# Optimization experiments

Hardware: AMD Instinct MI355X
Metric: run time of the kernel (lower is better)

## Reference

```python
import jax, jax.numpy as jnp
import numpy as np

B, S_DEC, S_ENC, D, H = 2, 2048, 2048, 1024, 16
HD = D // H  # 64


def setup_inputs() -> dict:
    key = jax.random.key(0)
    ks = jax.random.split(key, 12)
    s = 0.02
    return {
        "dec_hidden_state": jax.random.normal(ks[0], (B, S_DEC, D), jnp.float32),
        "enc_hidden_state": jax.random.normal(ks[1], (B, S_ENC, D), jnp.float32),
        "mask": jnp.ones((B, S_ENC, S_DEC), jnp.int32),
        "Wq": jax.random.normal(ks[2], (H, D, HD), jnp.float32) * s,
        "bq": jax.random.normal(ks[3], (H, HD), jnp.float32) * s,
        "Wk": jax.random.normal(ks[4], (H, D, HD), jnp.float32) * s,
        "bk": jax.random.normal(ks[5], (H, HD), jnp.float32) * s,
        "Wv": jax.random.normal(ks[6], (H, D, HD), jnp.float32) * s,
        "bv": jax.random.normal(ks[7], (H, HD), jnp.float32) * s,
        "Wo": jax.random.normal(ks[8], (D, D), jnp.float32) * s,
        "bo": jax.random.normal(ks[9], (D,), jnp.float32) * s,
    }


def reference(dec_hidden_state, enc_hidden_state, mask, Wq, bq, Wk, bk, Wv, bv, Wo, bo):
    # NOTE: original module swaps args: query <- enc_hidden_state, key/value <- dec_hidden_state.
    # q: [B,H,S_enc,HD], k/v: [B,H,S_dec,HD]
    q = jnp.einsum("bqd,hdk->bhqk", enc_hidden_state, Wq) + bq[None, :, None, :]
    k = jnp.einsum("bsd,hdk->bhsk", dec_hidden_state, Wk) + bk[None, :, None, :]
    v = jnp.einsum("bsd,hdk->bhsk", dec_hidden_state, Wv) + bv[None, :, None, :]
    scores = jnp.einsum("bhqk,bhsk->bhqs", q, k) / jnp.sqrt(jnp.asarray(HD, q.dtype))
    scores = jnp.where(mask[:, None, :, :] == 0, jnp.asarray(-jnp.inf, scores.dtype), scores)
    weights = jax.nn.softmax(scores, axis=-1)
    attn = jnp.einsum("bhqs,bhsk->bhqk", weights, v)  # [B,H,S_enc,HD]
    # concat heads along last dim (same order as torch.cat over head list)
    attn = jnp.transpose(attn, (0, 2, 1, 3)).reshape(B, S_ENC, D)
    return attn @ Wo + bo
```

## Files before the change

kernel.cpp:

```cpp
#include <hip/hip_runtime.h>
#include <math.h>
#include <stdint.h>


typedef unsigned short ushort_t;
typedef __attribute__((ext_vector_type(8))) short short8;
typedef __attribute__((ext_vector_type(4))) float floatx4;

__device__ __forceinline__ ushort_t f2bf(float x){
  unsigned u = __float_as_uint(x);
  u += 0x7fffu + ((u >> 16) & 1u);
  return (ushort_t)(u >> 16);
}
__device__ __forceinline__ unsigned pk2bf(float a, float b){
#if __has_builtin(__builtin_amdgcn_cvt_pk_bf16_f32)
  typedef __attribute__((ext_vector_type(2))) __bf16 bf2_t;
  bf2_t r = __builtin_amdgcn_cvt_pk_bf16_f32(a, b);
  return *(unsigned*)&r;
#else
  return (unsigned)f2bf(a) | ((unsigned)f2bf(b) << 16);
#endif
}
__device__ __forceinline__ floatx4 mfma16(short8 a, short8 b, floatx4 c){
  return __builtin_amdgcn_mfma_f32_16x16x32_bf16(a, b, c, 0, 0, 0);
}

__global__ __launch_bounds__(256)
void prep_kernel(const float* __restrict__ enc, const float* __restrict__ dec,
                 const float* __restrict__ Wq, const float* __restrict__ Wk,
                 const float* __restrict__ Wv, const float* __restrict__ Wo,
                 const int* __restrict__ mask,
                 ushort_t* __restrict__ encb, ushort_t* __restrict__ decb,
                 ushort_t* __restrict__ WqT, ushort_t* __restrict__ WkT,
                 ushort_t* __restrict__ WvT, ushort_t* __restrict__ WoT,
                 unsigned long long* __restrict__ mb)
{
  __shared__ float t[64][65];
  const int bx = blockIdx.x, tid = threadIdx.x;
  if (bx < 8192){
    const float* src = (bx < 4096) ? enc : dec;
    ushort_t*    dst = (bx < 4096) ? encb : decb;
    int i = ((bx & 4095) * 256 + tid) * 4;
    const float4 v = *(const float4*)(src + i);
    unsigned long long p = (unsigned long long)f2bf(v.x)
                         | ((unsigned long long)f2bf(v.y) << 16)
                         | ((unsigned long long)f2bf(v.z) << 32)
                         | ((unsigned long long)f2bf(v.w) << 48);
    *(unsigned long long*)(dst + i) = p;
  } else if (bx < 8960){
    const int id = bx - 8192;
    const int zz = id >> 4, yy = id & 15;
    const int which = zz >> 4, head = zz & 15;
    const float* src = (which == 0) ? Wq : (which == 1) ? Wk : Wv;
    ushort_t*    dst = (which == 0) ? WqT : (which == 1) ? WkT : WvT;
    const long sb = (long)head * 65536;
    const int r0 = yy * 64;
    #pragma unroll
    for (int i = 0; i < 16; i++){
      int idx = i*256 + tid;
      int r = idx >> 6, c = idx & 63;
      t[r][c] = src[sb + (long)(r0 + r)*64 + c];
    }
    __syncthreads();
    #pragma unroll
    for (int i = 0; i < 16; i++){
      int idx = i*256 + tid;
      int cr = idx >> 6, rc = idx & 63;
      dst[sb + (long)cr*1024 + r0 + rc] = f2bf(t[rc][cr]);
    }
  } else if (bx < 9216){
    const int id = bx - 8960;
    const int r0 = (id >> 4) * 64, c0 = (id & 15) * 64;
    #pragma unroll
    for (int i = 0; i < 16; i++){
      int idx = i*256 + tid;
      int r = idx >> 6, c = idx & 63;
      t[r][c] = Wo[(long)(r0 + r)*1024 + c0 + c];
    }
    __syncthreads();
    #pragma unroll
    for (int i = 0; i < 16; i++){
      int idx = i*256 + tid;
      int cr = idx >> 6, rc = idx & 63;
      WoT[(long)(c0 + cr)*1024 + r0 + rc] = f2bf(t[rc][cr]);
    }
  } else {
    long gid = (long)(bx - 9216) * 256 + tid;
    unsigned long long bal = __ballot(mask[gid] != 0);
    if ((tid & 63) == 0) mb[gid >> 6] = bal;
  }
}

__global__ __launch_bounds__(256, 3)
void gemm_qkv_kernel(const ushort_t* __restrict__ encb, const ushort_t* __restrict__ decb,
                     const ushort_t* __restrict__ WqT, const ushort_t* __restrict__ WkT,
                     const ushort_t* __restrict__ WvT,
                     const float* __restrict__ bq, const float* __restrict__ bk,
                     const float* __restrict__ bv,
                     ushort_t* __restrict__ Qb, ushort_t* __restrict__ Kbf,
                     ushort_t* __restrict__ Vtb)
{
  __shared__ ushort_t At[2*4096];
  __shared__ ushort_t Bt[2*4096];
  const int tid = threadIdx.x;
  const int wave = tid >> 6, lane = tid & 63;
  const int quad = lane >> 4, l16 = lane & 15;
  const int z = blockIdx.z;
  const ushort_t *A, *BT; const float* bias; ushort_t* outp;
  int m0, n0; long outAdj = 0;
  float qs = 1.0f;
  if (z == 0){ A = encb; BT = WqT; bias = bq; outp = Qb;  m0 = blockIdx.x*128; n0 = blockIdx.y*128;
               qs = 0.18033688011112042f; }
  else if (z == 1){ A = decb; BT = WkT; bias = bk; outp = Kbf; m0 = blockIdx.x*128; n0 = blockIdx.y*128; }
  else {
    int id = blockIdx.x*8 + blockIdx.y;
    int vb = id >> 7, rem = id & 127;
    m0 = ((rem >> 4) & 7) * 128; n0 = (rem & 15) * 128;
    A = WvT; BT = decb + (long)vb*2097152; bias = bv; outp = Vtb; outAdj = (long)vb*2097152;
  }
  const int K = 1024;

  const int c0 = tid, c1 = 256 + tid;
  const ushort_t* gA0 = A  + (long)(m0 + (c0 >> 2))*K + (c0 & 3)*8;
  const ushort_t* gA1 = A  + (long)(m0 + (c1 >> 2))*K + (c1 & 3)*8;
  const ushort_t* gB0 = BT + (long)(n0 + (c0 >> 2))*K + (c0 & 3)*8;
  const ushort_t* gB1 = BT + (long)(n0 + (c1 >> 2))*K + (c1 & 3)*8;

  floatx4 acc[4][4];
  #pragma unroll
  for (int mt = 0; mt < 4; mt++)
    #pragma unroll
    for (int nt = 0; nt < 4; nt++)
      acc[mt][nt] = (floatx4){0.f, 0.f, 0.f, 0.f};

  short8 rA0 = *(const short8*)gA0;  gA0 += 32;
  short8 rA1 = *(const short8*)gA1;  gA1 += 32;
  short8 rB0 = *(const short8*)gB0;  gB0 += 32;
  short8 rB1 = *(const short8*)gB1;  gB1 += 32;

  const int moff = (wave & 1) * 64, noff = (wave >> 1) * 64;
  int cur = 0;
  for (int k0 = 0; k0 < K; k0 += 32){
    *(short8*)&At[cur*4096 +        tid*8] = rA0;
    *(short8*)&At[cur*4096 + 2048 + tid*8] = rA1;
    *(short8*)&Bt[cur*4096 +        tid*8] = rB0;
    *(short8*)&Bt[cur*4096 + 2048 + tid*8] = rB1;
    __syncthreads();
    if (k0 + 32 < K){
      rA0 = *(const short8*)gA0;  gA0 += 32;
      rA1 = *(const short8*)gA1;  gA1 += 32;
      rB0 = *(const short8*)gB0;  gB0 += 32;
      rB1 = *(const short8*)gB1;  gB1 += 32;
    }
    short8 af[4], bfr[4];
    #pragma unroll
    for (int t = 0; t < 4; t++){
      af[t]  = *(const short8*)&At[cur*4096 + (moff + t*16 + l16)*32 + quad*8];
      bfr[t] = *(const short8*)&Bt[cur*4096 + (noff + t*16 + l16)*32 + quad*8];
    }
    #pragma unroll
    for (int mt = 0; mt < 4; mt++)
      #pragma unroll
      for (int nt = 0; nt < 4; nt++)
        acc[mt][nt] = mfma16(bfr[nt], af[mt], acc[mt][nt]);
    cur ^= 1;
  }

  #pragma unroll
  for (int mt = 0; mt < 4; mt++){
    #pragma unroll
    for (int nt = 0; nt < 4; nt++){
      floatx4 v = acc[mt][nt];
      if (z < 2){
        const int s   = m0 + moff + mt*16 + l16;
        const int ch0 = n0 + noff + nt*16 + quad*4;
        const float4 b4 = *(const float4*)&bias[ch0];
        uint2 pk;
        pk.x = pk2bf((v[0] + b4.x)*qs, (v[1] + b4.y)*qs);
        pk.y = pk2bf((v[2] + b4.z)*qs, (v[3] + b4.w)*qs);
        *(unsigned long long*)&outp[(long)s*1024 + ch0] = *(unsigned long long*)&pk;
      } else {
        const int ch = m0 + moff + mt*16 + l16;
        const int s0 = n0 + noff + nt*16 + quad*4;
        const float bb = bias[ch];
        uint2 pk;
        pk.x = pk2bf(v[0] + bb, v[1] + bb);
        pk.y = pk2bf(v[2] + bb, v[3] + bb);
        *(unsigned long long*)&outp[outAdj + (long)ch*2048 + s0] = *(unsigned long long*)&pk;
      }
    }
  }
}

__global__ __launch_bounds__(256, 2)
void gemm_o_kernel(const ushort_t* __restrict__ A, const ushort_t* __restrict__ BT,
                   const float* __restrict__ bias, float* __restrict__ outf)
{
  __shared__ ushort_t At[2*4096];
  __shared__ ushort_t Bt[2*2048];
  const int tid = threadIdx.x;
  const int wave = tid >> 6, lane = tid & 63;
  const int quad = lane >> 4, l16 = lane & 15;
  const int m0 = blockIdx.x * 128, n0 = blockIdx.y * 64;
  const int K = 1024;

  const int c0 = tid, c1 = 256 + tid;
  const ushort_t* gA0 = A  + (long)(m0 + (c0 >> 2))*K + (c0 & 3)*8;
  const ushort_t* gA1 = A  + (long)(m0 + (c1 >> 2))*K + (c1 & 3)*8;
  const ushort_t* gB0 = BT + (long)(n0 + (c0 >> 2))*K + (c0 & 3)*8;

  floatx4 acc[4][2];
  #pragma unroll
  for (int mt = 0; mt < 4; mt++)
    #pragma unroll
    for (int nt = 0; nt < 2; nt++)
      acc[mt][nt] = (floatx4){0.f, 0.f, 0.f, 0.f};

  short8 rA0 = *(const short8*)gA0;  gA0 += 32;
  short8 rA1 = *(const short8*)gA1;  gA1 += 32;
  short8 rB0 = *(const short8*)gB0;  gB0 += 32;

  const int moff = (wave & 1) * 64, noff = (wave >> 1) * 32;
  int cur = 0;
  for (int k0 = 0; k0 < K; k0 += 32){
    *(short8*)&At[cur*4096 +        tid*8] = rA0;
    *(short8*)&At[cur*4096 + 2048 + tid*8] = rA1;
    *(short8*)&Bt[cur*2048 +        tid*8] = rB0;
    __syncthreads();
    if (k0 + 32 < K){
      rA0 = *(const short8*)gA0;  gA0 += 32;
      rA1 = *(const short8*)gA1;  gA1 += 32;
      rB0 = *(const short8*)gB0;  gB0 += 32;
    }
    short8 af[4], bfr[2];
    #pragma unroll
    for (int t = 0; t < 4; t++)
      af[t]  = *(const short8*)&At[cur*4096 + (moff + t*16 + l16)*32 + quad*8];
    #pragma unroll
    for (int t = 0; t < 2; t++)
      bfr[t] = *(const short8*)&Bt[cur*2048 + (noff + t*16 + l16)*32 + quad*8];
    #pragma unroll
    for (int mt = 0; mt < 4; mt++)
      #pragma unroll
      for (int nt = 0; nt < 2; nt++)
        acc[mt][nt] = mfma16(bfr[nt], af[mt], acc[mt][nt]);
    cur ^= 1;
  }

  #pragma unroll
  for (int mt = 0; mt < 4; mt++){
    #pragma unroll
    for (int nt = 0; nt < 2; nt++){
      const int s   = m0 + moff + mt*16 + l16;
      const int ch0 = n0 + noff + nt*16 + quad*4;
      const float4 b4 = *(const float4*)&bias[ch0];
      float4 o;
      o.x = acc[mt][nt][0] + b4.x;
      o.y = acc[mt][nt][1] + b4.y;
      o.z = acc[mt][nt][2] + b4.z;
      o.w = acc[mt][nt][3] + b4.w;
      *(float4*)&outf[(long)s*1024 + ch0] = o;
    }
  }
}

#define SM_PB(zA_, zB_, wv_, lsum_, pb_)                              \
  {                                                                   \
    float p0 = __builtin_amdgcn_exp2f((zA_)[0]);                      \
    float p1 = __builtin_amdgcn_exp2f((zA_)[1]);                      \
    float p2 = __builtin_amdgcn_exp2f((zA_)[2]);                      \
    float p3 = __builtin_amdgcn_exp2f((zA_)[3]);                      \
    float p4 = __builtin_amdgcn_exp2f((zB_)[0]);                      \
    float p5 = __builtin_amdgcn_exp2f((zB_)[1]);                      \
    float p6 = __builtin_amdgcn_exp2f((zB_)[2]);                      \
    float p7 = __builtin_amdgcn_exp2f((zB_)[3]);                      \
    if (__builtin_expect(!uni, 0)){                                   \
      const int sh_ = quad*8;                                         \
      p0 = (((wv_) >> (sh_+0)) & 1u) ? p0 : 0.f;                      \
      p1 = (((wv_) >> (sh_+1)) & 1u) ? p1 : 0.f;                      \
      p2 = (((wv_) >> (sh_+2)) & 1u) ? p2 : 0.f;                      \
      p3 = (((wv_) >> (sh_+3)) & 1u) ? p3 : 0.f;                      \
      p4 = (((wv_) >> (sh_+4)) & 1u) ? p4 : 0.f;                      \
      p5 = (((wv_) >> (sh_+5)) & 1u) ? p5 : 0.f;                      \
      p6 = (((wv_) >> (sh_+6)) & 1u) ? p6 : 0.f;                      \
      p7 = (((wv_) >> (sh_+7)) & 1u) ? p7 : 0.f;                      \
    }                                                                 \
    lsum_ += ((p0 + p1) + (p2 + p3)) + ((p4 + p5) + (p6 + p7));       \
    unsigned pk0_ = pk2bf(p0, p1);                                    \
    unsigned pk1_ = pk2bf(p2, p3);                                    \
    unsigned pk2_ = pk2bf(p4, p5);                                    \
    unsigned pk3_ = pk2bf(p6, p7);                                    \
    unsigned tmp_[4] = {pk0_, pk1_, pk2_, pk3_};                      \
    __builtin_memcpy(&(pb_), tmp_, 16);                               \
  }

__global__ __launch_bounds__(512, 4)
void flash_attn_kernel(const ushort_t* __restrict__ Qp, const ushort_t* __restrict__ Kp,
                       const ushort_t* __restrict__ Vt, const unsigned* __restrict__ mb,
                       ushort_t* __restrict__ aout)
{
  __shared__ __align__(16) unsigned char smem_raw[73728];
  ushort_t* KBs = (ushort_t*)smem_raw;
  ushort_t* VBs = KBs + 2*2*4608;
  float* mO = (float*)smem_raw;
  float* mL = (float*)(smem_raw + 32768);

  const int tid = threadIdx.x, wave = tid >> 6, lane = tid & 63;
  const int quad = lane >> 4, l16 = lane & 15;
  const int shalf = wave >> 2, w = wave & 3;
  const int bh = blockIdx.x, qt = blockIdx.y;
  const int b = bh >> 4, h = bh & 15;

  const ushort_t* VB = Vt + (long)bh*131072;
  const int q0 = qt*128 + w*32;

  short8 qfA0, qfA1, qfB0, qfB1;
  {
    const long qrowA = ((long)b*2048 + q0 + l16)*1024 + h*64;
    qfA0 = *(const short8*)&Qp[qrowA +      quad*8];
    qfA1 = *(const short8*)&Qp[qrowA + 32 + quad*8];
    const long qrowB = qrowA + 16*1024;
    qfB0 = *(const short8*)&Qp[qrowB +      quad*8];
    qfB1 = *(const short8*)&Qp[qrowB + 32 + quad*8];
  }

  floatx4 accA[4], accB[4];
  #pragma unroll
  for (int ht = 0; ht < 4; ht++){
    accA[ht] = (floatx4){0.f,0.f,0.f,0.f};
    accB[ht] = (floatx4){0.f,0.f,0.f,0.f};
  }
  float lsA = 0.f, lsB = 0.f;

  const int htid = tid & 255;
  const int c0 = htid, c1 = 256 + htid;
  const int sr0 = c0 >> 3, sr1 = c1 >> 3;
  const int kr0 = (sr0 & 32) + ((sr0 & 4) << 2) + ((sr0 >> 3) & 3)*4 + (sr0 & 3);
  const int kr1 = (sr1 & 32) + ((sr1 & 4) << 2) + ((sr1 >> 3) & 3)*4 + (sr1 & 3);
  const long srow = (long)b*2048 + shalf*1024;
  const ushort_t* gK0 = Kp + (srow + sr0)*1024 + h*64 + (c0 & 7)*8;
  const ushort_t* gK1 = Kp + (srow + sr1)*1024 + h*64 + (c1 & 7)*8;
  const ushort_t* gV0 = VB + (long)sr0*2048 + shalf*1024 + (c0 & 7)*8;
  const ushort_t* gV1 = VB + (long)sr1*2048 + shalf*1024 + (c1 & 7)*8;
  ushort_t* Kh = KBs + shalf*2*4608;
  ushort_t* Vh = VBs + shalf*2*4608;
  const int ko0 = kr0*72 + (c0 & 7)*8;
  const int ko1 = kr1*72 + (c1 & 7)*8;
  const int vo0 = sr0*72 + (c0 & 7)*8;
  const int vo1 = sr1*72 + (c1 & 7)*8;

  const uint2* mb2 = (const uint2*)mb;
  const long mbase = (long)b*2048 + q0;

  short8 gk0 = *(const short8*)gK0;  gK0 += 65536;
  short8 gk1 = *(const short8*)gK1;  gK1 += 65536;
  short8 gv0 = *(const short8*)gV0;  gV0 += 64;
  short8 gv1 = *(const short8*)gV1;  gV1 += 64;

  int cur = 0;
  for (int st = 0; st < 16; st++){
    *(short8*)&Kh[cur*4608 + ko0] = gk0;
    *(short8*)&Kh[cur*4608 + ko1] = gk1;
    *(short8*)&Vh[cur*4608 + vo0] = gv0;
    *(short8*)&Vh[cur*4608 + vo1] = gv1;
    __syncthreads();
    if (st < 15){
      gk0 = *(const short8*)gK0;  gK0 += 65536;
      gk1 = *(const short8*)gK1;  gK1 += 65536;
      gv0 = *(const short8*)gV0;  gV0 += 64;
      gv1 = *(const short8*)gV1;  gV1 += 64;
    }
    const ushort_t* Kt = &Kh[cur*4608];
    const ushort_t* Vp = &Vh[cur*4608];

    const uint2 mwA = mb2[(mbase +      l16)*32 + shalf*16 + st];
    const uint2 mwB = mb2[(mbase + 16 + l16)*32 + shalf*16 + st];
    const bool uni = __all((mwA.x & mwA.y & mwB.x & mwB.y) == 0xFFFFFFFFu);

    #pragma unroll
    for (int c = 0; c < 2; c++){
      short8 kA0 = *(const short8*)&Kt[((c*2    )*16 + l16)*72 +      quad*8];
      short8 kA1 = *(const short8*)&Kt[((c*2    )*16 + l16)*72 + 32 + quad*8];
      short8 kB0 = *(const short8*)&Kt[((c*2 + 1)*16 + l16)*72 +      quad*8];
      short8 kB1 = *(const short8*)&Kt[((c*2 + 1)*16 + l16)*72 + 32 + quad*8];

      floatx4 zA = (floatx4){0.f,0.f,0.f,0.f};
      zA = mfma16(kA0, qfA0, zA);
      zA = mfma16(kA1, qfA1, zA);
      floatx4 zB = (floatx4){0.f,0.f,0.f,0.f};
      zB = mfma16(kB0, qfA0, zB);
      zB = mfma16(kB1, qfA1, zB);
      const unsigned wvA = c ? mwA.y : mwA.x;
      short8 pbA;
      SM_PB(zA, zB, wvA, lsA, pbA);

      zA = (floatx4){0.f,0.f,0.f,0.f};
      zA = mfma16(kA0, qfB0, zA);
      zA = mfma16(kA1, qfB1, zA);
      zB = (floatx4){0.f,0.f,0.f,0.f};
      zB = mfma16(kB0, qfB0, zB);
      zB = mfma16(kB1, qfB1, zB);
      const unsigned wvB = c ? mwB.y : mwB.x;
      short8 pbB;
      SM_PB(zA, zB, wvB, lsB, pbB);

      #pragma unroll
      for (int ht = 0; ht < 4; ht++){
        const short8 vf = *(const short8*)&Vp[(ht*16 + l16)*72 + c*32 + quad*8];
        accA[ht] = mfma16(vf, pbA, accA[ht]);
        accB[ht] = mfma16(vf, pbB, accB[ht]);
      }
    }
    cur ^= 1;
  }

  lsA += __shfl_xor(lsA, 16);
  lsA += __shfl_xor(lsA, 32);
  lsB += __shfl_xor(lsB, 16);
  lsB += __shfl_xor(lsB, 32);

  __syncthreads();
  if (shalf == 1){
    #pragma unroll
    for (int ht = 0; ht < 4; ht++){
      *(floatx4*)&mO[((((w*2 + 0)*4 + ht)*64) + lane)*4] = accA[ht];
      *(floatx4*)&mO[((((w*2 + 1)*4 + ht)*64) + lane)*4] = accB[ht];
    }
    mL[(w*2 + 0)*64 + lane] = lsA;
    mL[(w*2 + 1)*64 + lane] = lsB;
  }
  __syncthreads();
  if (shalf == 0){
    const float invA = 1.0f / (lsA + mL[(w*2 + 0)*64 + lane]);
    const float invB = 1.0f / (lsB + mL[(w*2 + 1)*64 + lane]);
    const long rowoA = ((long)b*2048 + q0 + l16)*1024 + h*64;
    const long rowoB = rowoA + 16*1024;
    #pragma unroll
    for (int ht = 0; ht < 4; ht++){
      const floatx4 oA = *(const floatx4*)&mO[((((w*2 + 0)*4 + ht)*64) + lane)*4];
      uint2 pkA;
      pkA.x = pk2bf((accA[ht][0] + oA[0])*invA, (accA[ht][1] + oA[1])*invA);
      pkA.y = pk2bf((accA[ht][2] + oA[2])*invA, (accA[ht][3] + oA[3])*invA);
      *(unsigned long long*)&aout[rowoA + ht*16 + quad*4] = *(unsigned long long*)&pkA;
      const floatx4 oB = *(const floatx4*)&mO[((((w*2 + 1)*4 + ht)*64) + lane)*4];
      uint2 pkB;
      pkB.x = pk2bf((accB[ht][0] + oB[0])*invB, (accB[ht][1] + oB[1])*invB);
      pkB.y = pk2bf((accB[ht][2] + oB[2])*invB, (accB[ht][3] + oB[3])*invB);
      *(unsigned long long*)&aout[rowoB + ht*16 + quad*4] = *(unsigned long long*)&pkB;
    }
  }
}

extern "C" void kernel_launch(void* const* d_in, const int* in_sizes, int n_in,
                              void* d_out, int out_size, void* d_ws, size_t ws_size,
                              hipStream_t stream) {
  const float* dec  = (const float*)d_in[0];
  const float* enc  = (const float*)d_in[1];
  const int*   mask = (const int*)d_in[2];
  const float* Wq   = (const float*)d_in[3];
  const float* bq   = (const float*)d_in[4];
  const float* Wk   = (const float*)d_in[5];
  const float* bk   = (const float*)d_in[6];
  const float* Wv   = (const float*)d_in[7];
  const float* bv   = (const float*)d_in[8];
  const float* Wo   = (const float*)d_in[9];
  const float* bo   = (const float*)d_in[10];
  float* out = (float*)d_out;

  ushort_t* ws   = (ushort_t*)d_ws;
  ushort_t* encb = ws;
  ushort_t* decb = encb + 4194304;
  ushort_t* Qb   = decb + 4194304;
  ushort_t* Kbf  = Qb   + 4194304;
  ushort_t* Vtb  = Kbf  + 4194304;
  ushort_t* WqT  = Vtb  + 4194304;
  ushort_t* WkT  = WqT  + 1048576;
  ushort_t* WvT  = WkT  + 1048576;
  ushort_t* WoT  = WvT  + 1048576;
  unsigned* Mb   = (unsigned*)(WoT + 1048576);

  prep_kernel<<<41984, 256, 0, stream>>>(enc, dec, Wq, Wk, Wv, Wo, mask,
                                         encb, decb, WqT, WkT, WvT, WoT,
                                         (unsigned long long*)Mb);
  gemm_qkv_kernel<<<dim3(32,8,3), 256, 0, stream>>>(encb, decb, WqT, WkT, WvT,
                                                    bq, bk, bv, Qb, Kbf, Vtb);
  flash_attn_kernel<<<dim3(32,16,1), 512, 0, stream>>>(Qb, Kbf, Vtb, Mb, encb);
  gemm_o_kernel<<<dim3(32,16,1), 256, 0, stream>>>(encb, WoT, bo, out);
}
```

Before: 272.4 us.

## Stream K/V tiles directly into LDS with XOR-swizzled unpadded layout

Replaces the register-staged global-to-LDS copy of K and V tiles with direct global_load_lds async loads into a double buffer, prefetching the next tile while computing the current one. The padded 72-element row layout becomes an unpadded 64-element layout with an XOR swizzle on the column group to avoid LDS bank conflicts. This shrinks shared memory and frees registers. In exchange it needs manual vmcnt/lgkmcnt waits and an extra barrier per iteration, which adds synchronization risk.

```diff
diff --git a/kernel.cpp b/kernel.cpp
--- a/kernel.cpp
+++ b/kernel.cpp
@@ -23,6 +23,10 @@
 }
 __device__ __forceinline__ floatx4 mfma16(short8 a, short8 b, floatx4 c){
   return __builtin_amdgcn_mfma_f32_16x16x32_bf16(a, b, c, 0, 0, 0);
+}
+__device__ __forceinline__ void gload16(const void* g, void* l){
+  __builtin_amdgcn_global_load_lds((const __attribute__((address_space(1))) void*)g,
+                                   (__attribute__((address_space(3))) void*)l, 16, 0, 0);
 }
 
 __global__ __launch_bounds__(256)
@@ -299,9 +303,9 @@
                        const ushort_t* __restrict__ Vt, const unsigned* __restrict__ mb,
                        ushort_t* __restrict__ aout)
 {
-  __shared__ __align__(16) unsigned char smem_raw[73728];
+  __shared__ __align__(16) unsigned char smem_raw[65536];
   ushort_t* KBs = (ushort_t*)smem_raw;
-  ushort_t* VBs = KBs + 2*2*4608;
+  ushort_t* VBs = KBs + 16384;
   float* mO = (float*)smem_raw;
   float* mL = (float*)(smem_raw + 32768);
 
@@ -313,6 +317,25 @@
 
   const ushort_t* VB = Vt + (long)bh*131072;
   const int q0 = qt*128 + w*32;
+
+  const int l8 = lane >> 3, cl = lane & 7;
+  const int r0 = w*16 + l8;
+  const int sr0 = (r0 & 35) | ((r0 & 4) << 1) | ((r0 & 16) >> 2);
+  const int cg = cl ^ l8;
+  const ushort_t* kp0 = Kp + ((long)b*2048 + shalf*1024 + sr0)*1024 + h*64 + cg*8;
+  const ushort_t* kp1 = kp0 + 16384;
+  const ushort_t* vp0 = VB + (long)r0*2048 + shalf*1024 + cg*8;
+  const ushort_t* vp1 = vp0 + 16384;
+  const int kdo = shalf*16384 + w*2048;
+  const int vdo = 32768 + shalf*16384 + w*2048;
+
+  {
+    char* kd = (char*)smem_raw + kdo;
+    gload16(kp0, kd); gload16(kp1, kd + 1024);
+    char* vd = (char*)smem_raw + vdo;
+    gload16(vp0, vd); gload16(vp1, vd + 1024);
+    kp0 += 65536; kp1 += 65536; vp0 += 64; vp1 += 64;
+  }
 
   short8 qfA0, qfA1, qfB0, qfB1;
   {
@@ -332,57 +355,42 @@
   }
   float lsA = 0.f, lsB = 0.f;
 
-  const int htid = tid & 255;
-  const int c0 = htid, c1 = 256 + htid;
-  const int sr0 = c0 >> 3, sr1 = c1 >> 3;
-  const int kr0 = (sr0 & 32) + ((sr0 & 4) << 2) + ((sr0 >> 3) & 3)*4 + (sr0 & 3);
-  const int kr1 = (sr1 & 32) + ((sr1 & 4) << 2) + ((sr1 >> 3) & 3)*4 + (sr1 & 3);
-  const long srow = (long)b*2048 + shalf*1024;
-  const ushort_t* gK0 = Kp + (srow + sr0)*1024 + h*64 + (c0 & 7)*8;
-  const ushort_t* gK1 = Kp + (srow + sr1)*1024 + h*64 + (c1 & 7)*8;
-  const ushort_t* gV0 = VB + (long)sr0*2048 + shalf*1024 + (c0 & 7)*8;
-  const ushort_t* gV1 = VB + (long)sr1*2048 + shalf*1024 + (c1 & 7)*8;
-  ushort_t* Kh = KBs + shalf*2*4608;
-  ushort_t* Vh = VBs + shalf*2*4608;
-  const int ko0 = kr0*72 + (c0 & 7)*8;
-  const int ko1 = kr1*72 + (c1 & 7)*8;
-  const int vo0 = sr0*72 + (c0 & 7)*8;
-  const int vo1 = sr1*72 + (c1 & 7)*8;
-
   const uint2* mb2 = (const uint2*)mb;
   const long mbase = (long)b*2048 + q0;
-
-  short8 gk0 = *(const short8*)gK0;  gK0 += 65536;
-  short8 gk1 = *(const short8*)gK1;  gK1 += 65536;
-  short8 gv0 = *(const short8*)gV0;  gV0 += 64;
-  short8 gv1 = *(const short8*)gV1;  gV1 += 64;
+  const int sw8 = l16 & 7;
+  const int kc0 = (quad ^ sw8) * 8;
+  const int kc1 = kc0 ^ 32;
 
   int cur = 0;
   for (int st = 0; st < 16; st++){
-    *(short8*)&Kh[cur*4608 + ko0] = gk0;
-    *(short8*)&Kh[cur*4608 + ko1] = gk1;
-    *(short8*)&Vh[cur*4608 + vo0] = gv0;
-    *(short8*)&Vh[cur*4608 + vo1] = gv1;
-    __syncthreads();
-    if (st < 15){
-      gk0 = *(const short8*)gK0;  gK0 += 65536;
-      gk1 = *(const short8*)gK1;  gK1 += 65536;
-      gv0 = *(const short8*)gV0;  gV0 += 64;
-      gv1 = *(const short8*)gV1;  gV1 += 64;
-    }
-    const ushort_t* Kt = &Kh[cur*4608];
-    const ushort_t* Vp = &Vh[cur*4608];
-
     const uint2 mwA = mb2[(mbase +      l16)*32 + shalf*16 + st];
     const uint2 mwB = mb2[(mbase + 16 + l16)*32 + shalf*16 + st];
+    __builtin_amdgcn_sched_barrier(0);
+    if (st < 15){
+      char* kd = (char*)smem_raw + kdo + (cur^1)*8192;
+      gload16(kp0, kd); gload16(kp1, kd + 1024);
+      char* vd = (char*)smem_raw + vdo + (cur^1)*8192;
+      gload16(vp0, vd); gload16(vp1, vd + 1024);
+      kp0 += 65536; kp1 += 65536; vp0 += 64; vp1 += 64;
+      asm volatile("s_waitcnt vmcnt(6)" ::: "memory");
+    } else {
+      asm volatile("s_waitcnt vmcnt(0)" ::: "memory");
+    }
+    __builtin_amdgcn_s_barrier();
+    __builtin_amdgcn_sched_barrier(0);
+
+    const ushort_t* Kt = KBs + shalf*8192 + cur*4096;
+    const ushort_t* Vp = VBs + shalf*8192 + cur*4096;
     const bool uni = __all((mwA.x & mwA.y & mwB.x & mwB.y) == 0xFFFFFFFFu);
 
     #pragma unroll
     for (int c = 0; c < 2; c++){
-      short8 kA0 = *(const short8*)&Kt[((c*2    )*16 + l16)*72 +      quad*8];
-      short8 kA1 = *(const short8*)&Kt[((c*2    )*16 + l16)*72 + 32 + quad*8];
-      short8 kB0 = *(const short8*)&Kt[((c*2 + 1)*16 + l16)*72 +      quad*8];
-      short8 kB1 = *(const short8*)&Kt[((c*2 + 1)*16 + l16)*72 + 32 + quad*8];
+      const int rA = (c*2    )*16 + l16;
+      const int rB = (c*2 + 1)*16 + l16;
+      short8 kA0 = *(const short8*)&Kt[rA*64 + kc0];
+      short8 kA1 = *(const short8*)&Kt[rA*64 + kc1];
+      short8 kB0 = *(const short8*)&Kt[rB*64 + kc0];
+      short8 kB1 = *(const short8*)&Kt[rB*64 + kc1];
 
       floatx4 zA = (floatx4){0.f,0.f,0.f,0.f};
       zA = mfma16(kA0, qfA0, zA);
@@ -404,13 +412,19 @@
       short8 pbB;
       SM_PB(zA, zB, wvB, lsB, pbB);
 
+      const int vcs = ((c*4 + quad) ^ sw8) * 8;
       #pragma unroll
       for (int ht = 0; ht < 4; ht++){
-        const short8 vf = *(const short8*)&Vp[(ht*16 + l16)*72 + c*32 + quad*8];
+        const short8 vf = *(const short8*)&Vp[(ht*16 + l16)*64 + vcs];
         accA[ht] = mfma16(vf, pbA, accA[ht]);
         accB[ht] = mfma16(vf, pbB, accB[ht]);
       }
     }
+
+    asm volatile("s_waitcnt lgkmcnt(0)" ::: "memory");
+    __builtin_amdgcn_sched_barrier(0);
+    __builtin_amdgcn_s_barrier();
+    __builtin_amdgcn_sched_barrier(0);
     cur ^= 1;
   }
 
```

Result: faster. 247.0 us (-9.3%).
